# Optimization experiments

Hardware: AMD Instinct MI355X
Metric: run time of the kernel (lower is better)

Reference implementation:

```python
import jax, jax.numpy as jnp
import numpy as np

N_HEADS = 8

def setup_inputs() -> dict:
    key = jax.random.key(0)
    ks = jax.random.split(key, 5)
    C = 256
    x = jax.random.normal(ks[0], (4, C, 48, 48), dtype=jnp.float32)
    w_qkv = jax.random.normal(ks[1], (3 * C, C), dtype=jnp.float32) * (C ** -0.5)
    b_qkv = jax.random.normal(ks[2], (3 * C,), dtype=jnp.float32) * 0.02
    w_proj = jax.random.normal(ks[3], (C, C), dtype=jnp.float32) * (C ** -0.5)
    b_proj = jax.random.normal(ks[4], (C,), dtype=jnp.float32) * 0.02
    return {"x": x, "w_qkv": w_qkv, "b_qkv": b_qkv, "w_proj": w_proj, "b_proj": b_proj}


def reference(x, w_qkv, b_qkv, w_proj, b_proj):
    B, C, H, W = x.shape
    h = N_HEADS
    dh = C // h
    N = H * W
    # flatten spatial dims to tokens: [B, N, C]
    xf = x.reshape(B, C, N).transpose(0, 2, 1)
    # fused qkv projection (torch Linear: y = x @ W.T + b)
    qkv = xf @ w_qkv.T + b_qkv                      # [B, N, 3C]
    qkv = qkv.reshape(B, N, 3, h, dh).transpose(2, 0, 3, 1, 4)  # [3, B, h, N, dh]
    q, k, v = qkv[0], qkv[1], qkv[2]
    scale = dh ** -0.5
    attn = jax.nn.softmax(jnp.einsum('bhnd,bhmd->bhnm', q, k) * scale, axis=-1)
    out = jnp.einsum('bhnm,bhmd->bhnd', attn, v)    # [B, h, N, dh]
    out = out.transpose(0, 2, 1, 3).reshape(B, N, C)
    out = out @ w_proj.T + b_proj                   # [B, N, C]
    return out.transpose(0, 2, 1).reshape(B, C, H, W)
```

## Files before the change

### kernel.cpp

```cpp
#include <hip/hip_runtime.h>
#include <hip/hip_bf16.h>

#define B_    4
#define C_    256
#define NTOK  2304
#define NH    8
#define DH    32

typedef short bf16x8 __attribute__((ext_vector_type(8)));
typedef short bf16x4 __attribute__((ext_vector_type(4)));
typedef float f32x4  __attribute__((ext_vector_type(4)));

__device__ __forceinline__ short rne_bf16(float f) {
    union { float f; unsigned u; } v; v.f = f;
    const unsigned r = v.u + 0x7fffu + ((v.u >> 16) & 1u);
    return (short)(r >> 16);
}
__device__ __forceinline__ unsigned pack2_bf16(float a, float b) {
    return (unsigned)(unsigned short)rne_bf16(a) | ((unsigned)(unsigned short)rne_bf16(b) << 16);
}
__device__ __forceinline__ float fast_exp2(float x) {
#if __has_builtin(__builtin_amdgcn_exp2f)
    return __builtin_amdgcn_exp2f(x);
#else
    return exp2f(x);
#endif
}

__global__ __launch_bounds__(256) void prep_kernel(
    const float* __restrict__ wq, const float* __restrict__ wp,
    short* __restrict__ wqb, short* __restrict__ wpb)
{
    const int id = blockIdx.x * 256 + threadIdx.x;
    const int base = id * 16;
    #pragma unroll
    for (int u = 0; u < 4; ++u) {
        const int off = base + u * 4;
        float4 v; short* d;
        if (off < 196608) { v = *(const float4*)(wq + off); d = wqb + off; }
        else { v = *(const float4*)(wp + (off - 196608)); d = wpb + (off - 196608); }
        d[0] = rne_bf16(v.x); d[1] = rne_bf16(v.y);
        d[2] = rne_bf16(v.z); d[3] = rne_bf16(v.w);
    }
}

__global__ __launch_bounds__(256) void qkv_mfma(
    const float* __restrict__ x,
    const short* __restrict__ wqb,
    const float* __restrict__ bias,
    short* __restrict__ qb, short* __restrict__ kb, short* __restrict__ vt)
{
    __shared__ short As[32][264];
    __shared__ short Es[4][2560];
    const int t    = threadIdx.x;
    const int wave = t >> 6;
    const int lane = t & 63;
    const int quad = lane >> 4, l16 = lane & 15;
    const int blk  = blockIdx.x;
    const int b    = blk / 216;
    const int rem  = blk % 216;
    const int mt   = rem / 3;
    const int jg   = rem % 3;
    const int m0   = mt * 32;
    const int j0   = (jg * 4 + wave) * 64;

    {
        const int n4  = (t & 7) * 4;
        const int tc2 = t >> 3;
        const float* xb = x + ((size_t)b * C_) * NTOK + m0 + n4;
        #pragma unroll
        for (int r = 0; r < 4; ++r) {
            const int c = tc2 * 2 + r * 64;
            const float4 v0 = *(const float4*)(xb + (size_t)c * NTOK);
            const float4 v1 = *(const float4*)(xb + (size_t)(c + 1) * NTOK);
            *(unsigned*)&As[n4 + 0][c] = pack2_bf16(v0.x, v1.x);
            *(unsigned*)&As[n4 + 1][c] = pack2_bf16(v0.y, v1.y);
            *(unsigned*)&As[n4 + 2][c] = pack2_bf16(v0.z, v1.z);
            *(unsigned*)&As[n4 + 3][c] = pack2_bf16(v0.w, v1.w);
        }
    }
    __syncthreads();

    const short* bbase = wqb + (size_t)(j0 + l16) * C_ + quad * 8;

    f32x4 acc[2][4] = {};
    for (int k0 = 0; k0 < C_; k0 += 32) {
        bf16x8 af[2], bfr[4];
        #pragma unroll
        for (int i = 0; i < 2; ++i)
            af[i] = *(const bf16x8*)&As[i * 16 + l16][k0 + quad * 8];
        #pragma unroll
        for (int j = 0; j < 4; ++j)
            bfr[j] = *(const bf16x8*)(bbase + (size_t)j * 16 * C_ + k0);
        #pragma unroll
        for (int i = 0; i < 2; ++i)
            #pragma unroll
            for (int j = 0; j < 4; ++j)
                acc[i][j] = __builtin_amdgcn_mfma_f32_16x16x32_bf16(af[i], bfr[j], acc[i][j], 0, 0, 0);
    }

    short* Ew = Es[wave];
    const int three = j0 >> 8;
    if (three < 2) {
        const float sc = (three == 0) ? 0.25503486f : 1.0f;
        #pragma unroll
        for (int j = 0; j < 4; ++j) {
            const float bv = bias[j0 + j * 16 + l16];
            #pragma unroll
            for (int i = 0; i < 2; ++i)
                #pragma unroll
                for (int r = 0; r < 4; ++r) {
                    const int n_l = i * 16 + quad * 4 + r;
                    Ew[n_l * 72 + j * 16 + l16] = rne_bf16((acc[i][j][r] + bv) * sc);
                }
        }
        const int n_l = lane & 31, hh = lane >> 5;
        const int head = ((j0 + hh * 32) >> 5) & 7;
        short* dst = ((three == 0) ? qb : kb)
                   + ((size_t)(b * NH + head) * NTOK + m0 + n_l) * DH;
        #pragma unroll
        for (int s = 0; s < 4; ++s)
            *(bf16x8*)(dst + s * 8) = *(const bf16x8*)&Ew[n_l * 72 + hh * 32 + s * 8];
    } else {
        #pragma unroll
        for (int j = 0; j < 4; ++j) {
            const float bv = bias[j0 + j * 16 + l16];
            const int j_l = j * 16 + l16;
            #pragma unroll
            for (int i = 0; i < 2; ++i) {
                const int nb = i * 16 + quad * 4;
                *(unsigned*)&Ew[j_l * 40 + nb] =
                    pack2_bf16(acc[i][j][0] + bv, acc[i][j][1] + bv);
                *(unsigned*)&Ew[j_l * 40 + nb + 2] =
                    pack2_bf16(acc[i][j][2] + bv, acc[i][j][3] + bv);
            }
        }
        #pragma unroll
        for (int p = 0; p < 4; ++p) {
            const int j_r = p * 16 + (lane >> 2);
            const int seg = (lane & 3) * 8;
            const int head = ((j0 + j_r) >> 5) & 7;
            const int d    = j_r & 31;
            *(bf16x8*)(vt + ((size_t)(b * NH + head) * DH + d) * NTOK + m0 + seg) =
                *(const bf16x8*)&Ew[j_r * 40 + seg];
        }
    }
}

__global__ __launch_bounds__(256) void attn_kernel(
    const short* __restrict__ qg,
    const short* __restrict__ kg,
    const short* __restrict__ vg,
    float* __restrict__ po,
    float* __restrict__ pl)
{
    const int bh   = blockIdx.y;
    const int q0   = blockIdx.x * 64;
    const int half = blockIdx.z;
    const int t    = threadIdx.x;
    const int wave = t >> 6;
    const int lane = t & 63;
    const int quad = lane >> 4;
    const int l16  = lane & 15;

    __shared__ short Ks[64][40];
    __shared__ short Vt[32][72];
    __shared__ short Ps[4][16][68];

    const short* kbase = kg + (size_t)bh * NTOK * DH;
    const short* vbase = vg + (size_t)bh * DH * NTOK;

    const short* qptr = qg + ((size_t)bh * NTOK + q0 + wave * 16 + l16) * DH + quad * 8;
    const bf16x8 qf = *(const bf16x8*)qptr;

    f32x4 Oc0 = {0.f, 0.f, 0.f, 0.f};
    f32x4 Oc1 = {0.f, 0.f, 0.f, 0.f};
    float lpart[4] = {0.f, 0.f, 0.f, 0.f};

    const int kbeg = half * (NTOK / 2);
    const int kend = kbeg + (NTOK / 2);

    const int kr = t >> 2, ksg = t & 3;
    const int vr = t >> 3, vsg = t & 7;

    bf16x8 kreg = *(const bf16x8*)(kbase + (size_t)(kbeg + kr) * DH + ksg * 8);
    bf16x8 vreg = *(const bf16x8*)(vbase + (size_t)vr * NTOK + kbeg + vsg * 8);

    for (int kt = kbeg; kt < kend; kt += 64) {
        *(bf16x8*)&Ks[kr][ksg * 8] = kreg;
        *(bf16x8*)&Vt[vr][vsg * 8] = vreg;
        __syncthreads();

        const int ktn = (kt + 64 < kend) ? kt + 64 : kbeg;
        kreg = *(const bf16x8*)(kbase + (size_t)(ktn + kr) * DH + ksg * 8);
        vreg = *(const bf16x8*)(vbase + (size_t)vr * NTOK + ktn + vsg * 8);

        f32x4 S[4];
        #pragma unroll
        for (int jt = 0; jt < 4; ++jt) {
            const bf16x8 kf = *(const bf16x8*)&Ks[jt * 16 + l16][quad * 8];
            f32x4 z = {0.f, 0.f, 0.f, 0.f};
            S[jt] = __builtin_amdgcn_mfma_f32_16x16x32_bf16(qf, kf, z, 0, 0, 0);
        }

        #pragma unroll
        for (int jt = 0; jt < 4; ++jt) {
            #pragma unroll
            for (int r = 0; r < 4; ++r) {
                const float p = fast_exp2(S[jt][r]);
                lpart[r] += p;
                Ps[wave][quad * 4 + r][jt * 16 + l16] = rne_bf16(p);
            }
        }

        #pragma unroll
        for (int jc = 0; jc < 2; ++jc) {
            const bf16x4 p0 = *(const bf16x4*)&Ps[wave][l16][jc * 32 + quad * 8];
            const bf16x4 p1 = *(const bf16x4*)&Ps[wave][l16][jc * 32 + quad * 8 + 4];
            bf16x8 af;
            af[0] = p0[0]; af[1] = p0[1]; af[2] = p0[2]; af[3] = p0[3];
            af[4] = p1[0]; af[5] = p1[1]; af[6] = p1[2]; af[7] = p1[3];
            const bf16x8 b0 = *(const bf16x8*)&Vt[l16][jc * 32 + quad * 8];
            const bf16x8 b1 = *(const bf16x8*)&Vt[16 + l16][jc * 32 + quad * 8];
            Oc0 = __builtin_amdgcn_mfma_f32_16x16x32_bf16(af, b0, Oc0, 0, 0, 0);
            Oc1 = __builtin_amdgcn_mfma_f32_16x16x32_bf16(af, b1, Oc1, 0, 0, 0);
        }
        __syncthreads();
    }

    #pragma unroll
    for (int off = 1; off < 16; off <<= 1) {
        #pragma unroll
        for (int r = 0; r < 4; ++r)
            lpart[r] += __shfl_xor(lpart[r], off, 64);
    }

    const size_t rowbase = ((size_t)half * 32 + bh) * NTOK + q0 + wave * 16 + quad * 4;
    float* obase = po + rowbase * DH + l16;
    #pragma unroll
    for (int r = 0; r < 4; ++r) {
        obase[(size_t)r * DH]      = Oc0[r];
        obase[(size_t)r * DH + 16] = Oc1[r];
    }
    if (l16 == 0) {
        float* lb = pl + rowbase;
        #pragma unroll
        for (int r = 0; r < 4; ++r) lb[r] = lpart[r];
    }
}

__global__ __launch_bounds__(256) void proj_mfma(
    const float* __restrict__ po,
    const float* __restrict__ pl,
    const short* __restrict__ wpb,
    const float* __restrict__ bias,
    float* __restrict__ out)
{
    __shared__ short Ac[32 * 336];
    __shared__ float Ep[4][2304];
    const int t    = threadIdx.x;
    const int wave = t >> 6;
    const int lane = t & 63;
    const int quad = lane >> 4, l16 = lane & 15;
    const int blk  = blockIdx.x;
    const int b    = blk / 72;
    const int mt   = blk % 72;
    const int m0   = mt * 32;
    const int c0   = wave * 64;

    const size_t PO_OFF = (size_t)32 * NTOK * DH;
    const size_t PL_OFF = (size_t)32 * NTOK;

    {
        const int m  = t >> 3;
        const int d4 = (t & 7) * 4;
        #pragma unroll
        for (int h = 0; h < NH; ++h) {
            const size_t row  = (size_t)(b * NH + h) * NTOK + m0 + m;
            const float inv = 1.f / (pl[row] + pl[PL_OFF + row]);
            const float* p0 = po + row * DH + d4;
            const f32x4 a = *(const f32x4*)p0;
            const f32x4 c = *(const f32x4*)(p0 + PO_OFF);
            short* dst = &Ac[m * 336 + h * 40 + d4];
            *(unsigned*)dst       = pack2_bf16((a[0] + c[0]) * inv, (a[1] + c[1]) * inv);
            *(unsigned*)(dst + 2) = pack2_bf16((a[2] + c[2]) * inv, (a[3] + c[3]) * inv);
        }
    }
    __syncthreads();

    const short* bbase = wpb + (size_t)(c0 + l16) * C_ + quad * 8;

    f32x4 acc[2][4] = {};
    for (int kt = 0; kt < 8; ++kt) {
        bf16x8 af[2], bfr[4];
        #pragma unroll
        for (int i = 0; i < 2; ++i)
            af[i] = *(const bf16x8*)&Ac[(i * 16 + l16) * 336 + kt * 40 + quad * 8];
        #pragma unroll
        for (int j = 0; j < 4; ++j)
            bfr[j] = *(const bf16x8*)(bbase + (size_t)j * 16 * C_ + kt * 32);
        #pragma unroll
        for (int i = 0; i < 2; ++i)
            #pragma unroll
            for (int j = 0; j < 4; ++j)
                acc[i][j] = __builtin_amdgcn_mfma_f32_16x16x32_bf16(af[i], bfr[j], acc[i][j], 0, 0, 0);
    }

    float* Ew = Ep[wave];
    #pragma unroll
    for (int j = 0; j < 4; ++j) {
        const int j_l = j * 16 + l16;
        const float bv = bias[c0 + j_l];
        #pragma unroll
        for (int i = 0; i < 2; ++i) {
            f32x4 st = {acc[i][j][0] + bv, acc[i][j][1] + bv,
                        acc[i][j][2] + bv, acc[i][j][3] + bv};
            *(f32x4*)&Ew[j_l * 36 + i * 16 + quad * 4] = st;
        }
    }
    #pragma unroll
    for (int p = 0; p < 8; ++p) {
        const int c_r = p * 8 + (lane >> 3);
        const int seg = (lane & 7) * 4;
        *(float4*)(out + ((size_t)b * C_ + c0 + c_r) * NTOK + m0 + seg) =
            *(const float4*)&Ew[c_r * 36 + seg];
    }
}

extern "C" void kernel_launch(void* const* d_in, const int* in_sizes, int n_in,
                              void* d_out, int out_size, void* d_ws, size_t ws_size,
                              hipStream_t stream) {
    const float* x      = (const float*)d_in[0];
    const float* w_qkv  = (const float*)d_in[1];
    const float* b_qkv  = (const float*)d_in[2];
    const float* w_proj = (const float*)d_in[3];
    const float* b_proj = (const float*)d_in[4];
    float* out = (float*)d_out;

    const size_t SZ = (size_t)B_ * NH * NTOK * DH;
    short* wqb = (short*)d_ws;
    short* wpb = wqb + 196608;
    short* qb  = wpb + 65536;
    short* kb  = qb + SZ;
    short* vt  = kb + SZ;
    float* po  = (float*)(vt + SZ);
    float* pl  = po + 2 * SZ;

    prep_kernel<<<64, 256, 0, stream>>>(w_qkv, w_proj, wqb, wpb);
    qkv_mfma<<<864, 256, 0, stream>>>(x, wqb, b_qkv, qb, kb, vt);
    attn_kernel<<<dim3(36, 32, 2), 256, 0, stream>>>(qb, kb, vt, po, pl);
    proj_mfma<<<288, 256, 0, stream>>>(po, pl, wpb, b_proj, out);
}
```

Before: 159.5 us.

## Use hardware bf16 packing, shrink GEMM tiles for more blocks, widen P loads

Switches bf16 rounding to the hardware packed-convert builtin when available and writes packed pairs in the weight prep kernel. The QKV GEMM now gives each wave 32 output columns (one head) instead of 64, doubling the grid to 1728 blocks. The projection GEMM now uses 16-token tiles, doubling its grid to 576 blocks. In attention, the P tile row stride is padded so the A fragment loads as one 16-byte read instead of two 8-byte reads. Smaller tiles give more parallelism and smaller LDS footprints, at the cost of lower per-block reuse of the x and weight loads.

```diff
diff --git a/kernel.cpp b/kernel.cpp
--- a/kernel.cpp
+++ b/kernel.cpp
@@ -11,6 +11,16 @@
 typedef short bf16x4 __attribute__((ext_vector_type(4)));
 typedef float f32x4  __attribute__((ext_vector_type(4)));
 
+#if __has_builtin(__builtin_amdgcn_cvt_pk_bf16_f32)
+__device__ __forceinline__ unsigned pack2_bf16(float a, float b) {
+    auto v = __builtin_amdgcn_cvt_pk_bf16_f32(a, b);
+    return __builtin_bit_cast(unsigned, v);
+}
+__device__ __forceinline__ short rne_bf16(float f) {
+    auto v = __builtin_amdgcn_cvt_pk_bf16_f32(f, f);
+    return (short)(__builtin_bit_cast(unsigned, v) & 0xffffu);
+}
+#else
 __device__ __forceinline__ short rne_bf16(float f) {
     union { float f; unsigned u; } v; v.f = f;
     const unsigned r = v.u + 0x7fffu + ((v.u >> 16) & 1u);
@@ -19,6 +29,7 @@
 __device__ __forceinline__ unsigned pack2_bf16(float a, float b) {
     return (unsigned)(unsigned short)rne_bf16(a) | ((unsigned)(unsigned short)rne_bf16(b) << 16);
 }
+#endif
 __device__ __forceinline__ float fast_exp2(float x) {
 #if __has_builtin(__builtin_amdgcn_exp2f)
     return __builtin_amdgcn_exp2f(x);
@@ -39,8 +50,8 @@
         float4 v; short* d;
         if (off < 196608) { v = *(const float4*)(wq + off); d = wqb + off; }
         else { v = *(const float4*)(wp + (off - 196608)); d = wpb + (off - 196608); }
-        d[0] = rne_bf16(v.x); d[1] = rne_bf16(v.y);
-        d[2] = rne_bf16(v.z); d[3] = rne_bf16(v.w);
+        *(unsigned*)d       = pack2_bf16(v.x, v.y);
+        *(unsigned*)(d + 2) = pack2_bf16(v.z, v.w);
     }
 }
 
@@ -51,18 +62,18 @@
     short* __restrict__ qb, short* __restrict__ kb, short* __restrict__ vt)
 {
     __shared__ short As[32][264];
-    __shared__ short Es[4][2560];
+    __shared__ short Es[4][1280];
     const int t    = threadIdx.x;
     const int wave = t >> 6;
     const int lane = t & 63;
     const int quad = lane >> 4, l16 = lane & 15;
     const int blk  = blockIdx.x;
-    const int b    = blk / 216;
-    const int rem  = blk % 216;
-    const int mt   = rem / 3;
-    const int jg   = rem % 3;
+    const int b    = blk / 432;
+    const int rem  = blk % 432;
+    const int mt   = rem / 6;
+    const int jg   = rem % 6;
     const int m0   = mt * 32;
-    const int j0   = (jg * 4 + wave) * 64;
+    const int j0   = jg * 128 + wave * 32;
 
     {
         const int n4  = (t & 7) * 4;
@@ -83,47 +94,49 @@
 
     const short* bbase = wqb + (size_t)(j0 + l16) * C_ + quad * 8;
 
-    f32x4 acc[2][4] = {};
+    f32x4 acc[2][2] = {};
     for (int k0 = 0; k0 < C_; k0 += 32) {
-        bf16x8 af[2], bfr[4];
+        bf16x8 af[2], bfr[2];
         #pragma unroll
         for (int i = 0; i < 2; ++i)
             af[i] = *(const bf16x8*)&As[i * 16 + l16][k0 + quad * 8];
         #pragma unroll
-        for (int j = 0; j < 4; ++j)
+        for (int j = 0; j < 2; ++j)
             bfr[j] = *(const bf16x8*)(bbase + (size_t)j * 16 * C_ + k0);
         #pragma unroll
         for (int i = 0; i < 2; ++i)
             #pragma unroll
-            for (int j = 0; j < 4; ++j)
+            for (int j = 0; j < 2; ++j)
                 acc[i][j] = __builtin_amdgcn_mfma_f32_16x16x32_bf16(af[i], bfr[j], acc[i][j], 0, 0, 0);
     }
 
     short* Ew = Es[wave];
-    const int three = j0 >> 8;
+    const int three = jg >> 1;
+    const int head  = (j0 >> 5) & 7;
     if (three < 2) {
         const float sc = (three == 0) ? 0.25503486f : 1.0f;
         #pragma unroll
-        for (int j = 0; j < 4; ++j) {
+        for (int j = 0; j < 2; ++j) {
             const float bv = bias[j0 + j * 16 + l16];
             #pragma unroll
             for (int i = 0; i < 2; ++i)
                 #pragma unroll
                 for (int r = 0; r < 4; ++r) {
                     const int n_l = i * 16 + quad * 4 + r;
-                    Ew[n_l * 72 + j * 16 + l16] = rne_bf16((acc[i][j][r] + bv) * sc);
+                    Ew[n_l * 40 + j * 16 + l16] = rne_bf16((acc[i][j][r] + bv) * sc);
                 }
         }
-        const int n_l = lane & 31, hh = lane >> 5;
-        const int head = ((j0 + hh * 32) >> 5) & 7;
+        const int n = lane >> 1;
         short* dst = ((three == 0) ? qb : kb)
-                   + ((size_t)(b * NH + head) * NTOK + m0 + n_l) * DH;
-        #pragma unroll
-        for (int s = 0; s < 4; ++s)
-            *(bf16x8*)(dst + s * 8) = *(const bf16x8*)&Ew[n_l * 72 + hh * 32 + s * 8];
+                   + ((size_t)(b * NH + head) * NTOK + m0 + n) * DH;
+        #pragma unroll
+        for (int s = 0; s < 2; ++s) {
+            const int off = (lane & 1) * 16 + s * 8;
+            *(bf16x8*)(dst + off) = *(const bf16x8*)&Ew[n * 40 + off];
+        }
     } else {
         #pragma unroll
-        for (int j = 0; j < 4; ++j) {
+        for (int j = 0; j < 2; ++j) {
             const float bv = bias[j0 + j * 16 + l16];
             const int j_l = j * 16 + l16;
             #pragma unroll
@@ -135,14 +148,12 @@
                     pack2_bf16(acc[i][j][2] + bv, acc[i][j][3] + bv);
             }
         }
-        #pragma unroll
-        for (int p = 0; p < 4; ++p) {
-            const int j_r = p * 16 + (lane >> 2);
-            const int seg = (lane & 3) * 8;
-            const int head = ((j0 + j_r) >> 5) & 7;
-            const int d    = j_r & 31;
-            *(bf16x8*)(vt + ((size_t)(b * NH + head) * DH + d) * NTOK + m0 + seg) =
-                *(const bf16x8*)&Ew[j_r * 40 + seg];
+        const int d = lane >> 1;
+        short* dst = vt + ((size_t)(b * NH + head) * DH + d) * NTOK + m0;
+        #pragma unroll
+        for (int s = 0; s < 2; ++s) {
+            const int off = (lane & 1) * 16 + s * 8;
+            *(bf16x8*)(dst + off) = *(const bf16x8*)&Ew[d * 40 + off];
         }
     }
 }
@@ -165,7 +176,7 @@
 
     __shared__ short Ks[64][40];
     __shared__ short Vt[32][72];
-    __shared__ short Ps[4][16][68];
+    __shared__ short Ps[4][16][72];
 
     const short* kbase = kg + (size_t)bh * NTOK * DH;
     const short* vbase = vg + (size_t)bh * DH * NTOK;
@@ -215,11 +226,7 @@
 
         #pragma unroll
         for (int jc = 0; jc < 2; ++jc) {
-            const bf16x4 p0 = *(const bf16x4*)&Ps[wave][l16][jc * 32 + quad * 8];
-            const bf16x4 p1 = *(const bf16x4*)&Ps[wave][l16][jc * 32 + quad * 8 + 4];
-            bf16x8 af;
-            af[0] = p0[0]; af[1] = p0[1]; af[2] = p0[2]; af[3] = p0[3];
-            af[4] = p1[0]; af[5] = p1[1]; af[6] = p1[2]; af[7] = p1[3];
+            const bf16x8 af = *(const bf16x8*)&Ps[wave][l16][jc * 32 + quad * 8];
             const bf16x8 b0 = *(const bf16x8*)&Vt[l16][jc * 32 + quad * 8];
             const bf16x8 b1 = *(const bf16x8*)&Vt[16 + l16][jc * 32 + quad * 8];
             Oc0 = __builtin_amdgcn_mfma_f32_16x16x32_bf16(af, b0, Oc0, 0, 0, 0);
@@ -256,54 +263,48 @@
     const float* __restrict__ bias,
     float* __restrict__ out)
 {
-    __shared__ short Ac[32 * 336];
-    __shared__ float Ep[4][2304];
+    __shared__ short Ac[16 * 336];
+    __shared__ float Ep[4][64 * 20];
     const int t    = threadIdx.x;
     const int wave = t >> 6;
     const int lane = t & 63;
     const int quad = lane >> 4, l16 = lane & 15;
     const int blk  = blockIdx.x;
-    const int b    = blk / 72;
-    const int mt   = blk % 72;
-    const int m0   = mt * 32;
+    const int b    = blk / 144;
+    const int mt   = blk % 144;
+    const int m0   = mt * 16;
     const int c0   = wave * 64;
 
     const size_t PO_OFF = (size_t)32 * NTOK * DH;
     const size_t PL_OFF = (size_t)32 * NTOK;
 
     {
-        const int m  = t >> 3;
-        const int d4 = (t & 7) * 4;
+        const int m   = t >> 4;
+        const int idx = t & 15;
         #pragma unroll
         for (int h = 0; h < NH; ++h) {
-            const size_t row  = (size_t)(b * NH + h) * NTOK + m0 + m;
+            const size_t row = (size_t)(b * NH + h) * NTOK + m0 + m;
             const float inv = 1.f / (pl[row] + pl[PL_OFF + row]);
-            const float* p0 = po + row * DH + d4;
-            const f32x4 a = *(const f32x4*)p0;
-            const f32x4 c = *(const f32x4*)(p0 + PO_OFF);
-            short* dst = &Ac[m * 336 + h * 40 + d4];
-            *(unsigned*)dst       = pack2_bf16((a[0] + c[0]) * inv, (a[1] + c[1]) * inv);
-            *(unsigned*)(dst + 2) = pack2_bf16((a[2] + c[2]) * inv, (a[3] + c[3]) * inv);
+            const float2 a = *(const float2*)(po + row * DH + idx * 2);
+            const float2 c = *(const float2*)(po + PO_OFF + row * DH + idx * 2);
+            *(unsigned*)&Ac[m * 336 + h * 40 + idx * 2] =
+                pack2_bf16((a.x + c.x) * inv, (a.y + c.y) * inv);
         }
     }
     __syncthreads();
 
     const short* bbase = wpb + (size_t)(c0 + l16) * C_ + quad * 8;
 
-    f32x4 acc[2][4] = {};
+    f32x4 acc[4] = {};
     for (int kt = 0; kt < 8; ++kt) {
-        bf16x8 af[2], bfr[4];
-        #pragma unroll
-        for (int i = 0; i < 2; ++i)
-            af[i] = *(const bf16x8*)&Ac[(i * 16 + l16) * 336 + kt * 40 + quad * 8];
+        const bf16x8 af = *(const bf16x8*)&Ac[l16 * 336 + kt * 40 + quad * 8];
+        bf16x8 bfr[4];
         #pragma unroll
         for (int j = 0; j < 4; ++j)
             bfr[j] = *(const bf16x8*)(bbase + (size_t)j * 16 * C_ + kt * 32);
         #pragma unroll
-        for (int i = 0; i < 2; ++i)
-            #pragma unroll
-            for (int j = 0; j < 4; ++j)
-                acc[i][j] = __builtin_amdgcn_mfma_f32_16x16x32_bf16(af[i], bfr[j], acc[i][j], 0, 0, 0);
+        for (int j = 0; j < 4; ++j)
+            acc[j] = __builtin_amdgcn_mfma_f32_16x16x32_bf16(af, bfr[j], acc[j], 0, 0, 0);
     }
 
     float* Ew = Ep[wave];
@@ -311,19 +312,16 @@
     for (int j = 0; j < 4; ++j) {
         const int j_l = j * 16 + l16;
         const float bv = bias[c0 + j_l];
-        #pragma unroll
-        for (int i = 0; i < 2; ++i) {
-            f32x4 st = {acc[i][j][0] + bv, acc[i][j][1] + bv,
-                        acc[i][j][2] + bv, acc[i][j][3] + bv};
-            *(f32x4*)&Ew[j_l * 36 + i * 16 + quad * 4] = st;
-        }
-    }
-    #pragma unroll
-    for (int p = 0; p < 8; ++p) {
-        const int c_r = p * 8 + (lane >> 3);
-        const int seg = (lane & 7) * 4;
+        f32x4 st = {acc[j][0] + bv, acc[j][1] + bv,
+                    acc[j][2] + bv, acc[j][3] + bv};
+        *(f32x4*)&Ew[j_l * 20 + quad * 4] = st;
+    }
+    #pragma unroll
+    for (int p = 0; p < 4; ++p) {
+        const int c_r = p * 16 + (lane >> 2);
+        const int seg = (lane & 3) * 4;
         *(float4*)(out + ((size_t)b * C_ + c0 + c_r) * NTOK + m0 + seg) =
-            *(const float4*)&Ew[c_r * 36 + seg];
+            *(const float4*)&Ew[c_r * 20 + seg];
     }
 }
 
@@ -347,7 +345,7 @@
     float* pl  = po + 2 * SZ;
 
     prep_kernel<<<64, 256, 0, stream>>>(w_qkv, w_proj, wqb, wpb);
-    qkv_mfma<<<864, 256, 0, stream>>>(x, wqb, b_qkv, qb, kb, vt);
+    qkv_mfma<<<1728, 256, 0, stream>>>(x, wqb, b_qkv, qb, kb, vt);
     attn_kernel<<<dim3(36, 32, 2), 256, 0, stream>>>(qb, kb, vt, po, pl);
-    proj_mfma<<<288, 256, 0, stream>>>(po, pl, wpb, b_proj, out);
-}
+    proj_mfma<<<576, 256, 0, stream>>>(po, pl, wpb, b_proj, out);
+}
```

Measured after the change: 164.0 us. 1.03x slower.
